# Kernel optimization log

Measured on AMD Instinct MI355X. Metric: run time of the kernel, lower is better.

The kernel has to match this reference:

```python
import jax, jax.numpy as jnp
import numpy as np

PAD = 0  # pad_token_id sentinel used for word_starts and labels_arcs masking


def setup_inputs() -> dict:
    B, S, H, L = 16, 256, 768, 37
    key = jax.random.key(0)
    k1, k2, k3, k4, k5 = jax.random.split(key, 5)
    hidden = jax.random.normal(k1, (B, S, H), dtype=jnp.float32)
    # strictly-increasing subword start indices (1,3,5,...), zero-padded to S
    n_starts = S // 2
    row = jnp.concatenate([
        1 + 2 * jnp.arange(n_starts, dtype=jnp.int32),
        jnp.zeros(S - n_starts, dtype=jnp.int32),
    ])
    word_starts = jnp.tile(row[None, :], (B, 1))
    n_words = n_starts - 1  # spans are between consecutive starts
    la = jax.random.randint(k2, (B, S), 1, 2 * S, dtype=jnp.int32)
    labels_arcs = jnp.where(jnp.arange(S)[None, :] < n_words, la, PAD)
    labels_rels = jax.random.randint(k3, (B, S), 0, L, dtype=jnp.int32)
    W_arc = jax.random.normal(k4, (H + 1, H), dtype=jnp.float32) * 0.02
    W_rel = jax.random.normal(k5, (L, H + 1, H + 1), dtype=jnp.float32) * 0.02
    return dict(hidden=hidden, W_arc=W_arc, W_rel=W_rel,
                word_starts=word_starts, labels_arcs=labels_arcs,
                labels_rels=labels_rels)


def _merge_subword_tokens(hidden, word_starts):
    """Fused segment-mean: word j = mean(hidden[start_j:start_{j+1}])."""
    B, S, H = hidden.shape
    csum = jnp.concatenate(
        [jnp.zeros((B, 1, H), hidden.dtype), jnp.cumsum(hidden, axis=1)], axis=1)
    n_valid = jnp.sum(word_starts != PAD, axis=1)  # [B]
    start = word_starts  # [B,S]
    end = jnp.concatenate(
        [word_starts[:, 1:], jnp.zeros((B, 1), word_starts.dtype)], axis=1)
    valid = (jnp.arange(S)[None, :] + 1) < n_valid[:, None]  # word j needs start j+1
    s0 = jnp.take_along_axis(csum, start[..., None].astype(jnp.int32), axis=1)
    s1 = jnp.take_along_axis(csum, end[..., None].astype(jnp.int32), axis=1)
    length = jnp.clip(end - start, 1, None).astype(hidden.dtype)[..., None]
    return jnp.where(valid[..., None], (s1 - s0) / length, 0.0)  # [B,S,H]


def _with_ones(x):
    return jnp.concatenate([x, jnp.ones_like(x[..., :1])], axis=-1)


def reference(hidden, W_arc, W_rel, word_starts, labels_arcs, labels_rels):
    deps = _merge_subword_tokens(hidden, word_starts)            # [B,S,H]
    heads = jnp.concatenate([hidden, deps], axis=1)              # [B,2S,H]
    xa = _with_ones(deps)                                        # [B,S,H+1]
    arc_preds = jnp.einsum('bxi,ij,byj->bxy', xa, W_arc, heads)  # [B,S,2S]
    yr = _with_ones(heads)                                       # [B,2S,H+1]
    rel_preds = jnp.einsum('bxi,oij,byj->bxyo', xa, W_rel, yr)   # [B,S,2S,L]

    B, S, Y, L = rel_preds.shape
    mask = (labels_arcs != PAD).astype(hidden.dtype)             # [B,S]
    n = jnp.sum(mask)
    arc_lp = jax.nn.log_softmax(arc_preds, axis=-1)
    safe_arcs = jnp.clip(labels_arcs, 0, Y - 1)
    arc_ll = jnp.take_along_axis(arc_lp, safe_arcs[..., None], axis=-1)[..., 0]
    arc_loss = -jnp.sum(arc_ll * mask) / n

    idx = jnp.broadcast_to(safe_arcs[:, :, None, None], (B, S, 1, L))
    rel_sel = jnp.take_along_axis(rel_preds, idx, axis=2)[:, :, 0, :]  # [B,S,L]
    rel_lp = jax.nn.log_softmax(rel_sel, axis=-1)
    rel_ll = jnp.take_along_axis(rel_lp, labels_rels[..., None], axis=-1)[..., 0]
    rel_loss = -jnp.sum(rel_ll * mask) / n

    loss = arc_loss + rel_loss
    return loss, rel_preds, arc_preds
```

## Files before the change

### kernel.cpp

```cpp
#include <hip/hip_runtime.h>
#include <cmath>
#include <cstdint>


#define NB 16
#define SS 256
#define HH 768
#define LLn 37
#define YY 512
#define KP 800
#define JP 896

static const long long REL_ELEMS = (long long)NB * SS * YY * LLn;
static const long long ARC_ELEMS = (long long)NB * SS * YY;

typedef __bf16 bf16_t;
typedef __bf16 bf16x8 __attribute__((ext_vector_type(8)));
typedef float f32x4 __attribute__((ext_vector_type(4)));

__device__ __forceinline__ void async_copy16(const void* g, void* l) {
  __builtin_amdgcn_global_load_lds((__attribute__((address_space(1))) void*)(g),
                                   (__attribute__((address_space(3))) void*)(l),
                                   16, 0, 0);
}


__global__ void count_valid(const int* __restrict__ word_starts,
                            int* __restrict__ n_valid, float* __restrict__ lossacc) {
  __shared__ int cnt;
  if (threadIdx.x == 0) cnt = 0;
  __syncthreads();
  const int b = blockIdx.x;
  if (word_starts[b * SS + threadIdx.x] != 0) atomicAdd(&cnt, 1);
  __syncthreads();
  if (threadIdx.x == 0) {
    n_valid[b] = cnt;
    if (b == 0) { lossacc[0] = 0.f; lossacc[1] = 0.f; }
  }
}

__global__ void hid_rows(const float* __restrict__ hidden, bf16_t* __restrict__ yrb) {
  const long long r = blockIdx.x;
  const int b = (int)(r >> 8), y = (int)(r & 255);
  const float* src = hidden + r * HH;
  bf16_t* dst = yrb + ((long long)b * YY + y) * KP;
  const int t = threadIdx.x;
  for (int h = t; h < HH; h += 256) dst[h] = (bf16_t)src[h];
  if (t < KP - HH) dst[HH + t] = (t == 0) ? (bf16_t)1.0f : (bf16_t)0.0f;
}

__global__ void build_deps(const float* __restrict__ hidden, const int* __restrict__ word_starts,
                           const int* __restrict__ n_valid,
                           bf16_t* __restrict__ xa_p, bf16_t* __restrict__ yrb) {
  const int x = blockIdx.x, b = blockIdx.y, t = threadIdx.x;
  const int nv = n_valid[b];
  const bool valid = (x + 1) < nv;
  int start = word_starts[b * SS + x];
  int end = (x + 1 < SS) ? word_starts[b * SS + x + 1] : 0;
  start = min(max(start, 0), SS); end = min(max(end, 0), SS);
  const int len = max(end - start, 1);
  const float inv = 1.0f / (float)len;
  const float* hb = hidden + (long long)b * SS * HH;
  bf16_t* xr = xa_p + (long long)(b * SS + x) * KP;
  bf16_t* yr = yrb + ((long long)b * YY + SS + x) * KP;
  for (int h = t; h < HH; h += 256) {
    float s = 0.f;
    if (valid) for (int tt = start; tt < end; ++tt) s += hb[(long long)tt * HH + h];
    const bf16_t bv = (bf16_t)(valid ? s * inv : 0.f);
    xr[h] = bv; yr[h] = bv;
  }
  if (t < KP - HH) {
    const bf16_t v = (t == 0) ? (bf16_t)1.0f : (bf16_t)0.0f;
    xr[HH + t] = v; yr[HH + t] = v;
  }
}

__global__ void conv_warc(const float* __restrict__ W, bf16_t* __restrict__ Wab) {
  __shared__ float tbuf[32][33];
  const int i0 = blockIdx.x * 32, j0 = blockIdx.y * 32;
  const int tx = threadIdx.x, ty = threadIdx.y;
  for (int rr = 0; rr < 32; rr += 8) {
    const int i = i0 + ty + rr, j = j0 + tx;
    tbuf[ty + rr][tx] = (i < HH + 1) ? W[(long long)i * HH + j] : 0.f;
  }
  __syncthreads();
  for (int rr = 0; rr < 32; rr += 8) {
    const int j = j0 + ty + rr, i = i0 + tx;
    Wab[(long long)j * KP + i] = (bf16_t)tbuf[tx][ty + rr];
  }
}

__global__ void conv_wrel(const float* __restrict__ W, bf16_t* __restrict__ Wb, int o0) {
  __shared__ float tbuf[32][33];
  const int o = o0 + blockIdx.z;
  const int i0 = blockIdx.x * 32, j0 = blockIdx.y * 32;
  const int tx = threadIdx.x, ty = threadIdx.y;
  const float* Wo = W + (long long)o * (HH + 1) * (HH + 1);
  for (int rr = 0; rr < 32; rr += 8) {
    const int i = i0 + ty + rr, j = j0 + tx;
    tbuf[ty + rr][tx] = (i < HH + 1 && j < HH + 1) ? Wo[(long long)i * (HH + 1) + j] : 0.f;
  }
  __syncthreads();
  bf16_t* Wbo = Wb + (long long)blockIdx.z * JP * KP;
  for (int rr = 0; rr < 32; rr += 8) {
    const int j = j0 + ty + rr, i = i0 + tx;
    Wbo[(long long)j * KP + i] = (bf16_t)tbuf[tx][ty + rr];
  }
}


__global__ __launch_bounds__(256)
void gemm_bt(const bf16_t* __restrict__ A, long long sAz, int lda,
             const bf16_t* __restrict__ B, long long sBz, int ldb,
             int K,
             float* __restrict__ Cf, bf16_t* __restrict__ Cb,
             long long sCz, int ldc,
             int mode, int OC, int o0) {
  __shared__ __align__(16) bf16_t As[128 * 32];
  __shared__ __align__(16) bf16_t Bs[128 * 32];
  const int tid = threadIdx.x;
  const int w = tid >> 6;
  const int lane = tid & 63;
  const int z = blockIdx.z;
  const long long row0 = (long long)blockIdx.y * 128;
  const long long col0 = (long long)blockIdx.x * 128;
  const bf16_t* Ab = A + z * sAz + row0 * lda;
  const bf16_t* Bb = B + z * sBz + col0 * ldb;

  const int r_in = lane >> 2;
  const int kofs = (lane & 3) * 8;
  const bf16_t* gA0 = Ab + (long long)(w * 32 + r_in) * lda + kofs;
  const bf16_t* gB0 = Bb + (long long)(w * 32 + r_in) * ldb + kofs;
  const bf16_t* gA1 = gA0 + 16ll * lda;
  const bf16_t* gB1 = gB0 + 16ll * ldb;
  bf16_t* lA0 = &As[(w * 32) * 32];
  bf16_t* lA1 = &As[(w * 32 + 16) * 32];
  bf16_t* lB0 = &Bs[(w * 32) * 32];
  bf16_t* lB1 = &Bs[(w * 32 + 16) * 32];

  f32x4 acc[4][4];
  #pragma unroll
  for (int i = 0; i < 4; i++)
    #pragma unroll
    for (int j = 0; j < 4; j++)
      #pragma unroll
      for (int e = 0; e < 4; e++) acc[i][j][e] = 0.f;

  const int wm = (w >> 1) * 64, wn = (w & 1) * 64;
  const int fr = lane & 15;
  const int fq = lane >> 4;
  const int aoff = fq * 8;

  for (int k0 = 0; k0 < K; k0 += 32) {
    async_copy16(gA0 + k0, lA0);
    async_copy16(gA1 + k0, lA1);
    async_copy16(gB0 + k0, lB0);
    async_copy16(gB1 + k0, lB1);
    __syncthreads();
    bf16x8 af[4], bfr[4];
    #pragma unroll
    for (int t = 0; t < 4; t++) af[t]  = *(const bf16x8*)&As[(wm + t * 16 + fr) * 32 + aoff];
    #pragma unroll
    for (int t = 0; t < 4; t++) bfr[t] = *(const bf16x8*)&Bs[(wn + t * 16 + fr) * 32 + aoff];
    #pragma unroll
    for (int tm = 0; tm < 4; tm++)
      #pragma unroll
      for (int tn = 0; tn < 4; tn++)
        acc[tm][tn] = __builtin_amdgcn_mfma_f32_16x16x32_bf16(af[tm], bfr[tn], acc[tm][tn], 0, 0, 0);
    __syncthreads();
  }

  const int er = fq * 4;
  #pragma unroll
  for (int tm = 0; tm < 4; tm++) {
    #pragma unroll
    for (int tn = 0; tn < 4; tn++) {
      const int rl = wm + tm * 16 + er;
      const long long col = col0 + wn + tn * 16 + fr;
      if (mode == 0) {
        bf16_t* dst = Cb + z * sCz + col;
        #pragma unroll
        for (int r = 0; r < 4; r++)
          dst[(row0 + rl + r) * (long long)ldc] = (bf16_t)acc[tm][tn][r];
      } else if (mode == 1) {
        float* dst = Cf + z * sCz + col;
        #pragma unroll
        for (int r = 0; r < 4; r++)
          dst[(row0 + rl + r) * (long long)ldc] = acc[tm][tn][r];
      } else {
        const int n = (int)col;
        const int x = n / OC;
        const int o = o0 + (n - x * OC);
        float* dst = Cf + z * sCz + (long long)x * (YY * LLn) + o;
        #pragma unroll
        for (int r = 0; r < 4; r++)
          dst[(row0 + rl + r) * (long long)LLn] = acc[tm][tn][r];
      }
    }
  }
}


__device__ __forceinline__ float wave_max(float v) {
  #pragma unroll
  for (int off = 32; off > 0; off >>= 1) v = fmaxf(v, __shfl_xor(v, off));
  return v;
}
__device__ __forceinline__ float wave_sum(float v) {
  #pragma unroll
  for (int off = 32; off > 0; off >>= 1) v += __shfl_xor(v, off);
  return v;
}

__global__ void loss_kernel(const float* __restrict__ arc, const float* __restrict__ rel,
                            const int* __restrict__ la, const int* __restrict__ lr,
                            float* __restrict__ acc) {
  const int r = blockIdx.x;
  const int lane = threadIdx.x;
  const int lab = la[r];
  const float* ar = arc + (long long)r * YY;
  float v[8]; float m = -INFINITY;
  #pragma unroll
  for (int i = 0; i < 8; i++) { v[i] = ar[lane + 64 * i]; m = fmaxf(m, v[i]); }
  m = wave_max(m);
  float s = 0.f;
  #pragma unroll
  for (int i = 0; i < 8; i++) s += expf(v[i] - m);
  s = wave_sum(s);
  const float lse_a = m + logf(s);
  const int safe = lab < 0 ? 0 : (lab > YY - 1 ? YY - 1 : lab);
  const float* rr = rel + ((long long)r * YY + safe) * LLn;
  const float rv = (lane < LLn) ? rr[lane] : -INFINITY;
  const float m2 = wave_max(rv);
  const float s2 = wave_sum((lane < LLn) ? expf(rv - m2) : 0.f);
  const float lse_r = m2 + logf(s2);
  if (lane == 0 && lab != 0) {
    const float ll = (ar[safe] - lse_a) + (rr[lr[r]] - lse_r);
    atomicAdd(&acc[0], ll);
    atomicAdd(&acc[1], 1.f);
  }
}

__global__ void finalize(const float* __restrict__ acc, float* __restrict__ out) {
  out[0] = -acc[0] / acc[1];
}


extern "C" void kernel_launch(void* const* d_in, const int* in_sizes, int n_in,
                              void* d_out, int out_size, void* d_ws, size_t ws_size,
                              hipStream_t stream) {
  (void)in_sizes; (void)n_in; (void)out_size;
  const float* hidden      = (const float*)d_in[0];
  const float* W_arc       = (const float*)d_in[1];
  const float* W_rel       = (const float*)d_in[2];
  const int* word_starts   = (const int*)d_in[3];
  const int* labels_arcs   = (const int*)d_in[4];
  const int* labels_rels   = (const int*)d_in[5];

  float* out = (float*)d_out;
  float* rel_out = out + 1;
  float* arc_out = rel_out + REL_ELEMS;

  char* ws = (char*)d_ws;
  int* n_valid = (int*)ws;
  float* lossacc = (float*)(ws + 64);
  bf16_t* xa_p = (bf16_t*)(ws + 256);
  bf16_t* yrb  = xa_p + (size_t)NB * SS * KP;
  bf16_t* Wab  = yrb + (size_t)NB * YY * KP;
  bf16_t* A1   = Wab + (size_t)HH * KP;
  bf16_t* Wbc  = A1 + (size_t)NB * SS * HH;

  const size_t fixedB = 256 + 2 * ((size_t)NB * SS * KP + (size_t)NB * YY * KP +
                                   (size_t)HH * KP + (size_t)NB * SS * HH);
  const size_t perOC = 2 * ((size_t)JP * KP + (size_t)NB * SS * JP);
  int OC = 1;
  if (ws_size > fixedB + perOC) {
    const size_t m = (ws_size - fixedB) / perOC;
    OC = (m > (size_t)LLn) ? LLn : (int)m;
  }
  bf16_t* M_p = Wbc + (size_t)OC * JP * KP;

  count_valid<<<NB, SS, 0, stream>>>(word_starts, n_valid, lossacc);
  hid_rows<<<NB * SS, 256, 0, stream>>>(hidden, yrb);
  build_deps<<<dim3(SS, NB), 256, 0, stream>>>(hidden, word_starts, n_valid, xa_p, yrb);
  conv_warc<<<dim3(25, 24), dim3(32, 8), 0, stream>>>(W_arc, Wab);

  gemm_bt<<<dim3(6, 32, 1), 256, 0, stream>>>(xa_p, 0, KP, Wab, 0, KP, KP,
                                              nullptr, A1, 0, HH, 0, 0, 0);
  gemm_bt<<<dim3(4, 2, NB), 256, 0, stream>>>(A1, (long long)SS * HH, HH,
                                              yrb, (long long)YY * KP, KP, HH,
                                              arc_out, nullptr, (long long)SS * YY, YY, 1, 0, 0);

  for (int o0 = 0; o0 < LLn; o0 += OC) {
    const int oc = (LLn - o0 < OC) ? (LLn - o0) : OC;
    conv_wrel<<<dim3(25, 28, oc), dim3(32, 8), 0, stream>>>(W_rel, Wbc, o0);
    gemm_bt<<<dim3(7, 32, oc), 256, 0, stream>>>(xa_p, 0, KP,
                                                 Wbc, (long long)JP * KP, KP, KP,
                                                 nullptr, M_p, JP, oc * JP, 0, 0, 0);
    gemm_bt<<<dim3(2 * oc, 4, NB), 256, 0, stream>>>(yrb, (long long)YY * KP, KP,
                                                     M_p, (long long)SS * oc * JP, JP, KP,
                                                     rel_out, nullptr, (long long)SS * YY * LLn,
                                                     0, 2, oc, o0);
  }

  loss_kernel<<<NB * SS, 64, 0, stream>>>(arc_out, rel_out, labels_arcs, labels_rels, lossacc);
  finalize<<<1, 1, 0, stream>>>(lossacc, out);
}
```

Measured before the change: 1.135 ms.

## Split W_rel bias column into separate GEMM and stage rel epilogue via LDS

The last column of W_rel (the ones-term of yr) is handled as a separate small GEMM producing a per-(x,o) bias, so the main rel GEMMs use J=768 instead of a padded 896 and K=768 in the second stage. The MODE-2 epilogue now goes through shared memory to write rows in a more coalesced pattern and adds the bias. gemm_bt is templated on mode. Together these cut redundant padded FLOPs and scattered stores, at the cost of an extra small kernel and more LDS use.

```diff
diff --git a/kernel.cpp b/kernel.cpp
--- a/kernel.cpp
+++ b/kernel.cpp
@@ -9,10 +9,9 @@
 #define LLn 37
 #define YY 512
 #define KP 800
-#define JP 896
+#define JR 768
 
 static const long long REL_ELEMS = (long long)NB * SS * YY * LLn;
-static const long long ARC_ELEMS = (long long)NB * SS * YY;
 
 typedef __bf16 bf16_t;
 typedef __bf16 bf16x8 __attribute__((ext_vector_type(8)));
@@ -98,26 +97,39 @@
   const float* Wo = W + (long long)o * (HH + 1) * (HH + 1);
   for (int rr = 0; rr < 32; rr += 8) {
     const int i = i0 + ty + rr, j = j0 + tx;
-    tbuf[ty + rr][tx] = (i < HH + 1 && j < HH + 1) ? Wo[(long long)i * (HH + 1) + j] : 0.f;
+    tbuf[ty + rr][tx] = (i < HH + 1) ? Wo[(long long)i * (HH + 1) + j] : 0.f;
   }
   __syncthreads();
-  bf16_t* Wbo = Wb + (long long)blockIdx.z * JP * KP;
+  bf16_t* Wbo = Wb + (long long)blockIdx.z * JR * KP;
   for (int rr = 0; rr < 32; rr += 8) {
     const int j = j0 + ty + rr, i = i0 + tx;
     Wbo[(long long)j * KP + i] = (bf16_t)tbuf[tx][ty + rr];
   }
 }
 
-
+__global__ void build_wb768(const float* __restrict__ W, bf16_t* __restrict__ Wb768) {
+  const int o = blockIdx.x;
+  bf16_t* dst = Wb768 + (long long)o * KP;
+  for (int i = threadIdx.x; i < KP; i += 256) {
+    float v = 0.f;
+    if (o < LLn && i < HH + 1)
+      v = W[(long long)o * (HH + 1) * (HH + 1) + (long long)i * (HH + 1) + HH];
+    dst[i] = (bf16_t)v;
+  }
+}
+
+
+template<int MODE>
 __global__ __launch_bounds__(256)
 void gemm_bt(const bf16_t* __restrict__ A, long long sAz, int lda,
              const bf16_t* __restrict__ B, long long sBz, int ldb,
              int K,
              float* __restrict__ Cf, bf16_t* __restrict__ Cb,
              long long sCz, int ldc,
-             int mode, int OC, int o0) {
-  __shared__ __align__(16) bf16_t As[128 * 32];
-  __shared__ __align__(16) bf16_t Bs[128 * 32];
+             int OC, int o0, const float* __restrict__ bias2) {
+  __shared__ __align__(16) char smem_raw[16896];
+  bf16_t* As = (bf16_t*)smem_raw;
+  bf16_t* Bs = (bf16_t*)(smem_raw + 8192);
   const int tid = threadIdx.x;
   const int w = tid >> 6;
   const int lane = tid & 63;
@@ -170,31 +182,48 @@
     __syncthreads();
   }
 
-  const int er = fq * 4;
-  #pragma unroll
-  for (int tm = 0; tm < 4; tm++) {
-    #pragma unroll
-    for (int tn = 0; tn < 4; tn++) {
-      const int rl = wm + tm * 16 + er;
-      const long long col = col0 + wn + tn * 16 + fr;
-      if (mode == 0) {
-        bf16_t* dst = Cb + z * sCz + col;
+  if (MODE == 2) {
+    float* ebuf = (float*)smem_raw;
+    const int c = tid & 127;
+    const int rgrp = tid >> 7;
+    const int n = (int)col0 + c;
+    const int x = n / OC;
+    const int o = o0 + (n - x * OC);
+    const float bias = bias2[(((long long)z << 8) + x) * 128 + o];
+    float* outp = Cf + z * sCz + (long long)x * (YY * LLn) + o;
+    #pragma unroll
+    for (int ch = 0; ch < 4; ch++) {
+      #pragma unroll
+      for (int tn = 0; tn < 4; tn++)
         #pragma unroll
-        for (int r = 0; r < 4; r++)
-          dst[(row0 + rl + r) * (long long)ldc] = (bf16_t)acc[tm][tn][r];
-      } else if (mode == 1) {
-        float* dst = Cf + z * sCz + col;
-        #pragma unroll
-        for (int r = 0; r < 4; r++)
-          dst[(row0 + rl + r) * (long long)ldc] = acc[tm][tn][r];
-      } else {
-        const int n = (int)col;
-        const int x = n / OC;
-        const int o = o0 + (n - x * OC);
-        float* dst = Cf + z * sCz + (long long)x * (YY * LLn) + o;
-        #pragma unroll
-        for (int r = 0; r < 4; r++)
-          dst[(row0 + rl + r) * (long long)LLn] = acc[tm][tn][r];
+        for (int e = 0; e < 4; e++)
+          ebuf[((w >> 1) * 16 + fq * 4 + e) * 132 + wn + tn * 16 + fr] = acc[ch][tn][e];
+      __syncthreads();
+      const long long ybase = row0 + (long long)rgrp * 64 + ch * 16;
+      #pragma unroll
+      for (int r = 0; r < 16; r++)
+        outp[(ybase + r) * LLn] = ebuf[(rgrp * 16 + r) * 132 + c] + bias;
+      __syncthreads();
+    }
+  } else {
+    const int er = fq * 4;
+    #pragma unroll
+    for (int tm = 0; tm < 4; tm++) {
+      #pragma unroll
+      for (int tn = 0; tn < 4; tn++) {
+        const int rl = wm + tm * 16 + er;
+        const long long col = col0 + wn + tn * 16 + fr;
+        if (MODE == 0) {
+          bf16_t* dst = Cb + z * sCz + col;
+          #pragma unroll
+          for (int r = 0; r < 4; r++)
+            dst[(row0 + rl + r) * (long long)ldc] = (bf16_t)acc[tm][tn][r];
+        } else {
+          float* dst = Cf + z * sCz + col;
+          #pragma unroll
+          for (int r = 0; r < 4; r++)
+            dst[(row0 + rl + r) * (long long)ldc] = acc[tm][tn][r];
+        }
       }
     }
   }
@@ -264,43 +293,52 @@
   char* ws = (char*)d_ws;
   int* n_valid = (int*)ws;
   float* lossacc = (float*)(ws + 64);
-  bf16_t* xa_p = (bf16_t*)(ws + 256);
-  bf16_t* yrb  = xa_p + (size_t)NB * SS * KP;
-  bf16_t* Wab  = yrb + (size_t)NB * YY * KP;
-  bf16_t* A1   = Wab + (size_t)HH * KP;
-  bf16_t* Wbc  = A1 + (size_t)NB * SS * HH;
+  bf16_t* xa_p  = (bf16_t*)(ws + 256);
+  bf16_t* yrb   = xa_p + (size_t)NB * SS * KP;
+  bf16_t* Wab   = yrb + (size_t)NB * YY * KP;
+  bf16_t* A1    = Wab + (size_t)HH * KP;
+  bf16_t* Wb768 = A1 + (size_t)NB * SS * HH;
+  float*  bias2 = (float*)(Wb768 + (size_t)128 * KP);
+  bf16_t* Wbc   = (bf16_t*)(bias2 + (size_t)NB * SS * 128);
 
   const size_t fixedB = 256 + 2 * ((size_t)NB * SS * KP + (size_t)NB * YY * KP +
-                                   (size_t)HH * KP + (size_t)NB * SS * HH);
-  const size_t perOC = 2 * ((size_t)JP * KP + (size_t)NB * SS * JP);
+                                   (size_t)HH * KP + (size_t)NB * SS * HH +
+                                   (size_t)128 * KP) +
+                        4 * (size_t)NB * SS * 128;
+  const size_t perOC = 2 * ((size_t)JR * KP + (size_t)NB * SS * JR);
   int OC = 1;
   if (ws_size > fixedB + perOC) {
     const size_t m = (ws_size - fixedB) / perOC;
     OC = (m > (size_t)LLn) ? LLn : (int)m;
   }
-  bf16_t* M_p = Wbc + (size_t)OC * JP * KP;
+  bf16_t* M_p = Wbc + (size_t)OC * JR * KP;
 
   count_valid<<<NB, SS, 0, stream>>>(word_starts, n_valid, lossacc);
   hid_rows<<<NB * SS, 256, 0, stream>>>(hidden, yrb);
   build_deps<<<dim3(SS, NB), 256, 0, stream>>>(hidden, word_starts, n_valid, xa_p, yrb);
   conv_warc<<<dim3(25, 24), dim3(32, 8), 0, stream>>>(W_arc, Wab);
-
-  gemm_bt<<<dim3(6, 32, 1), 256, 0, stream>>>(xa_p, 0, KP, Wab, 0, KP, KP,
-                                              nullptr, A1, 0, HH, 0, 0, 0);
-  gemm_bt<<<dim3(4, 2, NB), 256, 0, stream>>>(A1, (long long)SS * HH, HH,
-                                              yrb, (long long)YY * KP, KP, HH,
-                                              arc_out, nullptr, (long long)SS * YY, YY, 1, 0, 0);
+  build_wb768<<<128, 256, 0, stream>>>(W_rel, Wb768);
+
+  gemm_bt<0><<<dim3(6, 32, 1), 256, 0, stream>>>(xa_p, 0, KP, Wab, 0, KP, KP,
+                                                 nullptr, A1, 0, HH, 0, 0, nullptr);
+  gemm_bt<1><<<dim3(4, 2, NB), 256, 0, stream>>>(A1, (long long)SS * HH, HH,
+                                                 yrb, (long long)YY * KP, KP, HH,
+                                                 arc_out, nullptr, (long long)SS * YY, YY,
+                                                 0, 0, nullptr);
+  gemm_bt<1><<<dim3(1, 32, 1), 256, 0, stream>>>(xa_p, 0, KP, Wb768, 0, KP, KP,
+                                                 bias2, nullptr, 0, 128, 0, 0, nullptr);
 
   for (int o0 = 0; o0 < LLn; o0 += OC) {
     const int oc = (LLn - o0 < OC) ? (LLn - o0) : OC;
-    conv_wrel<<<dim3(25, 28, oc), dim3(32, 8), 0, stream>>>(W_rel, Wbc, o0);
-    gemm_bt<<<dim3(7, 32, oc), 256, 0, stream>>>(xa_p, 0, KP,
-                                                 Wbc, (long long)JP * KP, KP, KP,
-                                                 nullptr, M_p, JP, oc * JP, 0, 0, 0);
-    gemm_bt<<<dim3(2 * oc, 4, NB), 256, 0, stream>>>(yrb, (long long)YY * KP, KP,
-                                                     M_p, (long long)SS * oc * JP, JP, KP,
-                                                     rel_out, nullptr, (long long)SS * YY * LLn,
-                                                     0, 2, oc, o0);
+    conv_wrel<<<dim3(25, 24, oc), dim3(32, 8), 0, stream>>>(W_rel, Wbc, o0);
+    gemm_bt<0><<<dim3(6, 32, oc), 256, 0, stream>>>(xa_p, 0, KP,
+                                                    Wbc, (long long)JR * KP, KP, KP,
+                                                    nullptr, M_p, JR, oc * JR, 0, 0, nullptr);
+    gemm_bt<2><<<dim3(2 * oc, 4, NB), 256, 0, stream>>>(yrb, (long long)YY * KP, KP,
+                                                        M_p, (long long)SS * oc * JR, JR, JR,
+                                                        rel_out, nullptr,
+                                                        (long long)SS * YY * LLn, 0,
+                                                        oc, o0, bias2);
   }
 
   loss_kernel<<<NB * SS, 64, 0, stream>>>(arc_out, rel_out, labels_arcs, labels_rels, lossacc);
```

Measured after the change: 1.082 ms. -4.6%, faster.
